# Kernel tuning notes

Measured on AMD Instinct MI355X. Metric: run time of the kernel, lower is better.

The kernel has to match this reference:

```python
import jax, jax.numpy as jnp
import numpy as np

EPS = 1e-06


def setup_inputs() -> dict:
    key = jax.random.key(0)
    k1, k2, k3 = jax.random.split(key, 3)
    B, H, S, D = 4, 16, 4096, 64
    query = jax.random.normal(k1, (B, H, S, D), dtype=jnp.float32)
    key_t = jax.random.normal(k2, (B, H, S, D), dtype=jnp.float32)
    value = jax.random.normal(k3, (B, H, S, D), dtype=jnp.float32)
    return {"query": query, "key": key_t, "value": value}


def _cosformer_features(x, cos_idx, sin_idx):
    # x: [B,H,S,D]; cos_idx/sin_idx: [S,1] -> features [B,H,S,2D]
    x_relu = jax.nn.relu(x)
    return jnp.concatenate([x_relu * cos_idx, x_relu * sin_idx], axis=-1)


def reference(query, key, value):
    B, H, S, D = query.shape
    query = query / jnp.sqrt(jnp.asarray(D, dtype=query.dtype))
    # idx = (pi/2) * [1..S]; angles divided by seq_len
    ang = (jnp.pi / 2) * jnp.arange(1, S + 1, dtype=query.dtype) / S  # [S]
    cos_idx = jnp.cos(ang)[:, None]  # [S,1]
    sin_idx = jnp.sin(ang)[:, None]  # [S,1]
    q_cs = _cosformer_features(query, cos_idx, sin_idx)  # [B,H,S,2D]
    k_cs = _cosformer_features(key, cos_idx, sin_idx)    # [B,H,S,2D]
    # norm: 1 / clamp(q_cs . sum_l(k_cs), eps)
    k_sum = jnp.sum(k_cs, axis=-2)  # [B,H,2D]
    norm = 1.0 / jnp.maximum(jnp.einsum('bhld,bhd->bhl', q_cs, k_sum), EPS)  # [B,H,S]
    # linear attention: KV aggregation then query projection
    kv = jnp.einsum('bhld,bhlm->bhdm', k_cs, value)  # [B,H,2D,D]
    out = jnp.einsum('bhld,bhdm->bhlm', q_cs, kv) * norm[..., None]  # [B,H,S,D]
    return out
```

## Files before the change

kernel.cpp:

```cpp
#include <hip/hip_runtime.h>
#include <hip/hip_bf16.h>
#include <math.h>

#define BHN    64
#define SEQ    4096
#define DIM    64
#define NCHUNK 8
#define CHUNK  (SEQ / NCHUNK)
#define KSTEP  64
#define NIT    (CHUNK / KSTEP)
#define KVF    (128 * DIM)
#define STRIDE_C ((size_t)BHN * KVF + (size_t)BHN * 128)
#define KSBASE ((size_t)BHN * KVF)
#define FRAGH  10240
#define LPAD   72

typedef __bf16 bf16x8v __attribute__((ext_vector_type(8)));
typedef float  f32x4v  __attribute__((ext_vector_type(4)));

__device__ inline f32x4v mfma16(bf16x8v a, bf16x8v b, f32x4v c) {
    return __builtin_amdgcn_mfma_f32_16x16x32_bf16(a, b, c, 0, 0, 0);
}

__device__ inline unsigned pk2(float a, float b) {
    __hip_bfloat162 t(__float2bfloat16(a), __float2bfloat16(b));
    return *(unsigned*)&t;
}

__device__ __forceinline__ void barrier_noflush() {
    asm volatile("s_waitcnt lgkmcnt(0)" ::: "memory");
    __builtin_amdgcn_s_barrier();
    asm volatile("" ::: "memory");
}

__device__ inline int swz(int d, int col) { return col ^ (4 * ((d >> 2) & 7)); }

template<int USE_ATOMIC>
__global__ __launch_bounds__(512, 2) void cosformer_kv_mfma(
    const float* __restrict__ K, const float* __restrict__ V,
    float* __restrict__ part)
{
    __shared__ ushort ktc[64][LPAD];
    __shared__ ushort kts[64][LPAD];
    __shared__ ushort vtt[64][LPAD];

    const int bh    = blockIdx.x / NCHUNK;
    const int chunk = blockIdx.x % NCHUNK;
    const int row0  = chunk * CHUNK;
    const float* Kb = K + (size_t)bh * SEQ * DIM;
    const float* Vb = V + (size_t)bh * SEQ * DIM;

    const int tid = threadIdx.x;
    const int dq = (tid & 15) * 4;
    const int g  = tid >> 4;
    const int lane = tid & 63;
    const int w    = tid >> 6;
    const int frow = lane & 15;
    const int kgrp = lane >> 4;

    f32x4v acc[5];
    #pragma unroll
    for (int t = 0; t < 5; ++t) acc[t] = (f32x4v){0.f, 0.f, 0.f, 0.f};

    bf16x8v onef;
    #pragma unroll
    for (int j = 0; j < 8; ++j) onef[j] = (frow == 0) ? (__bf16)1.0f : (__bf16)0.0f;

    float4 sA[4], sB[4], sC[4], sD[4], sE[4], sF[4], sG[4], sH[4];

    auto LOADS = [&](int it, float4* r) {
        const float* kp = Kb + (size_t)(row0 + it * KSTEP + 2 * g) * DIM + dq;
        const float* vp = Vb + (size_t)(row0 + it * KSTEP + 2 * g) * DIM + dq;
        r[0] = *(const float4*)kp;
        r[1] = *(const float4*)(kp + DIM);
        r[2] = *(const float4*)vp;
        r[3] = *(const float4*)(vp + DIM);
    };

    auto WRITES = [&](int it, const float4* r) {
        const int l0 = row0 + it * KSTEP + 2 * g;
        const float CC = 1.5707963267948966f / (float)SEQ;
        float s0v, c0, s1v, c1;
        __sincosf(CC * (float)(l0 + 1), &s0v, &c0);
        __sincosf(CC * (float)(l0 + 2), &s1v, &c1);
        float k0[4] = {r[0].x, r[0].y, r[0].z, r[0].w};
        float k1[4] = {r[1].x, r[1].y, r[1].z, r[1].w};
        float v0[4] = {r[2].x, r[2].y, r[2].z, r[2].w};
        float v1[4] = {r[3].x, r[3].y, r[3].z, r[3].w};
        #pragma unroll
        for (int i = 0; i < 4; ++i) {
            const int d = dq + i;
            const int c = swz(d, g);
            float r0 = fmaxf(k0[i], 0.f), r1 = fmaxf(k1[i], 0.f);
            ((unsigned*)&ktc[d][0])[c] = pk2(r0 * c0,  r1 * c1);
            ((unsigned*)&kts[d][0])[c] = pk2(r0 * s0v, r1 * s1v);
            ((unsigned*)&vtt[d][0])[c] = pk2(v0[i],    v1[i]);
        }
    };

    LOADS(0, sA); LOADS(1, sB); LOADS(2, sC); LOADS(3, sD);
    LOADS(4, sE); LOADS(5, sF); LOADS(6, sG); LOADS(7, sH);

    const int d0 = (w & 3) * 16 + frow;

    #pragma unroll
    for (int it = 0; it < NIT; ++it) {
        if      (it == 0) WRITES(0, sA);
        else if (it == 1) WRITES(1, sB);
        else if (it == 2) WRITES(2, sC);
        else if (it == 3) WRITES(3, sD);
        else if (it == 4) WRITES(4, sE);
        else if (it == 5) WRITES(5, sF);
        else if (it == 6) WRITES(6, sG);
        else              WRITES(7, sH);
        barrier_noflush();

        const ushort (*ap)[LPAD] = (w < 4) ? ktc : kts;
        #pragma unroll
        for (int ks = 0; ks < 2; ++ks) {
            const int cb = ks * 16 + kgrp * 4;
            bf16x8v a = *(const bf16x8v*)&ap[d0][2 * swz(d0, cb)];
            #pragma unroll
            for (int nt = 0; nt < 4; ++nt) {
                const int dn = nt * 16 + frow;
                bf16x8v b = *(const bf16x8v*)&vtt[dn][2 * swz(dn, cb)];
                acc[nt] = mfma16(a, b, acc[nt]);
            }
            acc[4] = mfma16(a, onef, acc[4]);
        }
        barrier_noflush();
    }

    const int fb = w * 16 + kgrp * 4;
    if (USE_ATOMIC) {
        float* pb = part + (size_t)bh * KVF;
        float* ps = part + KSBASE + bh * 128;
        #pragma unroll
        for (int nt = 0; nt < 4; ++nt)
            #pragma unroll
            for (int r = 0; r < 4; ++r)
                atomicAdd(&pb[(size_t)(fb + r) * DIM + nt * 16 + frow], acc[nt][r]);
        if (frow == 0)
            #pragma unroll
            for (int r = 0; r < 4; ++r) atomicAdd(&ps[fb + r], acc[4][r]);
    } else {
        float* pb = part + STRIDE_C * chunk + (size_t)bh * KVF;
        float* ps = part + STRIDE_C * chunk + KSBASE + bh * 128;
        #pragma unroll
        for (int nt = 0; nt < 4; ++nt)
            #pragma unroll
            for (int r = 0; r < 4; ++r)
                pb[(size_t)(fb + r) * DIM + nt * 16 + frow] = acc[nt][r];
        if (frow == 0)
            #pragma unroll
            for (int r = 0; r < 4; ++r) ps[fb + r] = acc[4][r];
    }
}

template<int NC>
__global__ __launch_bounds__(256) void reduce_pack(
    const float* __restrict__ part, __hip_bfloat16* __restrict__ bfrag)
{
    size_t o = (size_t)blockIdx.x * 256 + threadIdx.x;
    float s = 0.f;
    #pragma unroll
    for (int c = 0; c < NC; ++c) s += part[(size_t)c * STRIDE_C + o];
    if (o < KSBASE) {
        int head = (int)(o >> 13);
        int r = (int)(o & 8191);
        int k = r >> 6, n = r & 63;
        int t = n >> 4, ks = k >> 5, lg = (k >> 3) & 3, j = k & 7;
        int lane = lg * 16 + (n & 15);
        bfrag[(size_t)head * FRAGH + (size_t)(((t * 4 + ks) * 64 + lane) * 8 + j)] =
            __float2bfloat16(s);
    } else {
        int r = (int)(o - KSBASE);
        int head = r >> 7, k = r & 127;
        int ks = k >> 5, lg = (k >> 3) & 3, j = k & 7;
        bfrag[(size_t)head * FRAGH + (size_t)(((16 + ks) * 64 + lg * 16) * 8 + j)] =
            __float2bfloat16(s);
    }
}

__global__ __launch_bounds__(256) void cosformer_out_mfma(
    const float* __restrict__ Q, const __hip_bfloat16* __restrict__ bfrag,
    float* __restrict__ out)
{
    __shared__ __hip_bfloat16 sb[FRAGH];
    const int head = blockIdx.x >> 3;
    const int tile = blockIdx.x & 7;
    const int tid  = threadIdx.x;

    {
        const float4* src = (const float4*)(bfrag + (size_t)head * FRAGH);
        float4* dst = (float4*)sb;
        #pragma unroll
        for (int i = 0; i < 5; ++i) dst[tid + 256 * i] = src[tid + 256 * i];
    }

    const int lane = tid & 63;
    const int w    = tid >> 6;
    const int mrow = lane & 15;
    const int kgrp = lane >> 4;

    const float* Qb = Q + (size_t)head * SEQ * DIM;
    float*       Ob = out + (size_t)head * SEQ * DIM;
    const int rowblk = tile * 512;

    float4 qb[2][4];
    #pragma unroll
    for (int m = 0; m < 2; ++m) {
        const float4* qr = (const float4*)(Qb + (size_t)(rowblk + w * 32 + m * 16 + mrow) * DIM);
        qb[m][0] = qr[kgrp * 2];
        qb[m][1] = qr[kgrp * 2 + 1];
        qb[m][2] = qr[8 + kgrp * 2];
        qb[m][3] = qr[8 + kgrp * 2 + 1];
    }

    barrier_noflush();

    #pragma unroll
    for (int g = 0; g < 4; ++g) {
        const int base = rowblk + (g * 4 + w) * 32;

        bf16x8v af[2][4];
        #pragma unroll
        for (int m = 0; m < 2; ++m) {
            int arow = base + m * 16 + mrow;
            float ang = 1.5707963267948966f * (float)(arow + 1) / (float)SEQ;
            float sn, cn;
            __sincosf(ang, &sn, &cn);
            float crs = cn * 0.125f, srs = sn * 0.125f;
            float lo[8] = {qb[m][0].x, qb[m][0].y, qb[m][0].z, qb[m][0].w,
                           qb[m][1].x, qb[m][1].y, qb[m][1].z, qb[m][1].w};
            float hi[8] = {qb[m][2].x, qb[m][2].y, qb[m][2].z, qb[m][2].w,
                           qb[m][3].x, qb[m][3].y, qb[m][3].z, qb[m][3].w};
            #pragma unroll
            for (int j = 0; j < 8; ++j) {
                float rl = fmaxf(lo[j], 0.f);
                float rh = fmaxf(hi[j], 0.f);
                af[m][0][j] = (__bf16)(rl * crs);
                af[m][1][j] = (__bf16)(rh * crs);
                af[m][2][j] = (__bf16)(rl * srs);
                af[m][3][j] = (__bf16)(rh * srs);
            }
        }

        if (g < 3) {
            #pragma unroll
            for (int m = 0; m < 2; ++m) {
                const float4* qr = (const float4*)(Qb + (size_t)(rowblk + ((g + 1) * 4 + w) * 32 + m * 16 + mrow) * DIM);
                qb[m][0] = qr[kgrp * 2];
                qb[m][1] = qr[kgrp * 2 + 1];
                qb[m][2] = qr[8 + kgrp * 2];
                qb[m][3] = qr[8 + kgrp * 2 + 1];
            }
        }

        f32x4v acc[2][5];
        #pragma unroll
        for (int m = 0; m < 2; ++m)
            #pragma unroll
            for (int t = 0; t < 5; ++t)
                acc[m][t] = (f32x4v){0.f, 0.f, 0.f, 0.f};

        #pragma unroll
        for (int t = 0; t < 5; ++t)
            #pragma unroll
            for (int ks = 0; ks < 4; ++ks) {
                bf16x8v bf = *(const bf16x8v*)&sb[(size_t)(((t * 4 + ks) * 64 + lane) * 8)];
                acc[0][t] = mfma16(af[0][ks], bf, acc[0][t]);
                acc[1][t] = mfma16(af[1][ks], bf, acc[1][t]);
            }

        #pragma unroll
        for (int m = 0; m < 2; ++m) {
            #pragma unroll
            for (int r = 0; r < 4; ++r) {
                float den = __shfl(acc[m][4][r], lane & 48, 64);
                float invd = 1.0f / fmaxf(den, 1e-6f);
                int row = base + m * 16 + kgrp * 4 + r;
                float* op = Ob + (size_t)row * DIM + mrow;
                op[0]  = acc[m][0][r] * invd;
                op[16] = acc[m][1][r] * invd;
                op[32] = acc[m][2][r] * invd;
                op[48] = acc[m][3][r] * invd;
            }
        }
    }
}

extern "C" void kernel_launch(void* const* d_in, const int* in_sizes, int n_in,
                              void* d_out, int out_size, void* d_ws, size_t ws_size,
                              hipStream_t stream) {
    const float* Q = (const float*)d_in[0];
    const float* K = (const float*)d_in[1];
    const float* V = (const float*)d_in[2];
    float* out = (float*)d_out;
    float* ws  = (float*)d_ws;

    const size_t frag_bytes = (size_t)FRAGH * BHN * sizeof(__hip_bfloat16);
    const size_t need_full  = (size_t)NCHUNK * STRIDE_C * sizeof(float) + frag_bytes;

    if (ws_size >= need_full) {
        float* part = ws;
        __hip_bfloat16* bfrag = (__hip_bfloat16*)(ws + (size_t)NCHUNK * STRIDE_C);
        hipMemsetAsync(bfrag, 0, frag_bytes, stream);
        hipLaunchKernelGGL((cosformer_kv_mfma<0>), dim3(BHN * NCHUNK), dim3(512), 0, stream,
                           K, V, part);
        hipLaunchKernelGGL((reduce_pack<NCHUNK>), dim3((int)(STRIDE_C / 256)), dim3(256), 0, stream,
                           part, bfrag);
        hipLaunchKernelGGL(cosformer_out_mfma, dim3(BHN * 8), dim3(256), 0, stream,
                           Q, bfrag, out);
    } else {
        float* part = ws;
        __hip_bfloat16* bfrag = (__hip_bfloat16*)(ws + STRIDE_C);
        hipMemsetAsync(part, 0, STRIDE_C * sizeof(float), stream);
        hipMemsetAsync(bfrag, 0, frag_bytes, stream);
        hipLaunchKernelGGL((cosformer_kv_mfma<1>), dim3(BHN * NCHUNK), dim3(512), 0, stream,
                           K, V, part);
        hipLaunchKernelGGL((reduce_pack<1>), dim3((int)(STRIDE_C / 256)), dim3(256), 0, stream,
                           part, bfrag);
        hipLaunchKernelGGL(cosformer_out_mfma, dim3(BHN * 8), dim3(256), 0, stream,
                           Q, bfrag, out);
    }
}
```

Measured before the change: 76.82 us.

## Stage K/V tiles via async global-to-LDS loads with triple buffering

Replaces the register-prefetch of all eight 64-row K/V tiles with direct global_load_lds copies into a three-slot LDS ring of 32-row raw fp32 tiles, issued two iterations ahead. Half the threads now transform K into cos/sin features and half convert V, each into transposed bf16 LDS tiles. The loop is no longer unrolled, and the trailing barrier is dropped in favour of one barrier after staging and one after the transform. The aim is to cut register pressure and overlap the memory loads with compute. In exchange it uses much more LDS, halves the work per barrier, and drops the occupancy hint of two blocks per CU.

```diff
diff --git a/kernel.cpp b/kernel.cpp
--- a/kernel.cpp
+++ b/kernel.cpp
@@ -1,19 +1,20 @@
 #include <hip/hip_runtime.h>
 #include <hip/hip_bf16.h>
 #include <math.h>
+#include <stdint.h>
 
 #define BHN    64
 #define SEQ    4096
 #define DIM    64
 #define NCHUNK 8
 #define CHUNK  (SEQ / NCHUNK)
-#define KSTEP  64
+#define KSTEP  32
 #define NIT    (CHUNK / KSTEP)
 #define KVF    (128 * DIM)
 #define STRIDE_C ((size_t)BHN * KVF + (size_t)BHN * 128)
 #define KSBASE ((size_t)BHN * KVF)
 #define FRAGH  10240
-#define LPAD   72
+#define LPADT  40
 
 typedef __bf16 bf16x8v __attribute__((ext_vector_type(8)));
 typedef float  f32x4v  __attribute__((ext_vector_type(4)));
@@ -33,16 +34,23 @@
     asm volatile("" ::: "memory");
 }
 
-__device__ inline int swz(int d, int col) { return col ^ (4 * ((d >> 2) & 7)); }
+__device__ __forceinline__ void gload16(const float* g, const float* lds_base) {
+    __builtin_amdgcn_global_load_lds(
+        (const __attribute__((address_space(1))) void*)(uintptr_t)g,
+        (__attribute__((address_space(3)))  void*)(uintptr_t)lds_base,
+        16, 0, 0);
+}
 
 template<int USE_ATOMIC>
-__global__ __launch_bounds__(512, 2) void cosformer_kv_mfma(
+__global__ __launch_bounds__(512) void cosformer_kv_mfma(
     const float* __restrict__ K, const float* __restrict__ V,
     float* __restrict__ part)
 {
-    __shared__ ushort ktc[64][LPAD];
-    __shared__ ushort kts[64][LPAD];
-    __shared__ ushort vtt[64][LPAD];
+    __shared__ float  rawK[3][KSTEP][DIM];
+    __shared__ float  rawV[3][KSTEP][DIM];
+    __shared__ ushort ktc[DIM][LPADT];
+    __shared__ ushort kts[DIM][LPADT];
+    __shared__ ushort vtt[DIM][LPADT];
 
     const int bh    = blockIdx.x / NCHUNK;
     const int chunk = blockIdx.x % NCHUNK;
@@ -50,13 +58,15 @@
     const float* Kb = K + (size_t)bh * SEQ * DIM;
     const float* Vb = V + (size_t)bh * SEQ * DIM;
 
-    const int tid = threadIdx.x;
-    const int dq = (tid & 15) * 4;
-    const int g  = tid >> 4;
+    const int tid  = threadIdx.x;
     const int lane = tid & 63;
     const int w    = tid >> 6;
+    const int g2    = (tid >> 4) & 15;
+    const int dq    = (tid & 15) * 4;
+    const int kvsel = tid >> 8;
     const int frow = lane & 15;
     const int kgrp = lane >> 4;
+    const int d0   = (w & 3) * 16 + frow;
 
     f32x4v acc[5];
     #pragma unroll
@@ -66,69 +76,76 @@
     #pragma unroll
     for (int j = 0; j < 8; ++j) onef[j] = (frow == 0) ? (__bf16)1.0f : (__bf16)0.0f;
 
-    float4 sA[4], sB[4], sC[4], sD[4], sE[4], sF[4], sG[4], sH[4];
-
-    auto LOADS = [&](int it, float4* r) {
-        const float* kp = Kb + (size_t)(row0 + it * KSTEP + 2 * g) * DIM + dq;
-        const float* vp = Vb + (size_t)(row0 + it * KSTEP + 2 * g) * DIM + dq;
-        r[0] = *(const float4*)kp;
-        r[1] = *(const float4*)(kp + DIM);
-        r[2] = *(const float4*)vp;
-        r[3] = *(const float4*)(vp + DIM);
+    auto STAGE = [&](int it) {
+        const int buf = it % 3;
+        const size_t go = (size_t)(row0 + it * KSTEP) * DIM + w * 256 + lane * 4;
+        gload16(Kb + go, &rawK[buf][w * 4][0]);
+        gload16(Vb + go, &rawV[buf][w * 4][0]);
     };
 
-    auto WRITES = [&](int it, const float4* r) {
-        const int l0 = row0 + it * KSTEP + 2 * g;
-        const float CC = 1.5707963267948966f / (float)SEQ;
-        float s0v, c0, s1v, c1;
-        __sincosf(CC * (float)(l0 + 1), &s0v, &c0);
-        __sincosf(CC * (float)(l0 + 2), &s1v, &c1);
-        float k0[4] = {r[0].x, r[0].y, r[0].z, r[0].w};
-        float k1[4] = {r[1].x, r[1].y, r[1].z, r[1].w};
-        float v0[4] = {r[2].x, r[2].y, r[2].z, r[2].w};
-        float v1[4] = {r[3].x, r[3].y, r[3].z, r[3].w};
-        #pragma unroll
-        for (int i = 0; i < 4; ++i) {
-            const int d = dq + i;
-            const int c = swz(d, g);
-            float r0 = fmaxf(k0[i], 0.f), r1 = fmaxf(k1[i], 0.f);
-            ((unsigned*)&ktc[d][0])[c] = pk2(r0 * c0,  r1 * c1);
-            ((unsigned*)&kts[d][0])[c] = pk2(r0 * s0v, r1 * s1v);
-            ((unsigned*)&vtt[d][0])[c] = pk2(v0[i],    v1[i]);
+    auto TRANSFORM = [&](int it) {
+        const int buf = it % 3;
+        const int r = 2 * g2;
+        if (kvsel == 0) {
+            float4 k0 = *(const float4*)&rawK[buf][r][dq];
+            float4 k1 = *(const float4*)&rawK[buf][r + 1][dq];
+            const int l0 = row0 + it * KSTEP + r;
+            const float CC = 1.5707963267948966f / (float)SEQ;
+            float s0v, c0, s1v, c1;
+            __sincosf(CC * (float)(l0 + 1), &s0v, &c0);
+            __sincosf(CC * (float)(l0 + 2), &s1v, &c1);
+            float a0[4] = {k0.x, k0.y, k0.z, k0.w};
+            float a1[4] = {k1.x, k1.y, k1.z, k1.w};
+            #pragma unroll
+            for (int i = 0; i < 4; ++i) {
+                const int d = dq + i;
+                const int c = g2 ^ (4 * ((d >> 2) & 3));
+                float r0 = fmaxf(a0[i], 0.f), r1 = fmaxf(a1[i], 0.f);
+                ((unsigned*)&ktc[d][0])[c] = pk2(r0 * c0,  r1 * c1);
+                ((unsigned*)&kts[d][0])[c] = pk2(r0 * s0v, r1 * s1v);
+            }
+        } else {
+            float4 v0q = *(const float4*)&rawV[buf][r][dq];
+            float4 v1q = *(const float4*)&rawV[buf][r + 1][dq];
+            float a0[4] = {v0q.x, v0q.y, v0q.z, v0q.w};
+            float a1[4] = {v1q.x, v1q.y, v1q.z, v1q.w};
+            #pragma unroll
+            for (int i = 0; i < 4; ++i) {
+                const int d = dq + i;
+                const int c = g2 ^ (4 * ((d >> 2) & 3));
+                ((unsigned*)&vtt[d][0])[c] = pk2(a0[i], a1[i]);
+            }
         }
     };
 
-    LOADS(0, sA); LOADS(1, sB); LOADS(2, sC); LOADS(3, sD);
-    LOADS(4, sE); LOADS(5, sF); LOADS(6, sG); LOADS(7, sH);
-
-    const int d0 = (w & 3) * 16 + frow;
-
-    #pragma unroll
+    STAGE(0);
+    STAGE(1);
+
+    #pragma unroll 1
     for (int it = 0; it < NIT; ++it) {
-        if      (it == 0) WRITES(0, sA);
-        else if (it == 1) WRITES(1, sB);
-        else if (it == 2) WRITES(2, sC);
-        else if (it == 3) WRITES(3, sD);
-        else if (it == 4) WRITES(4, sE);
-        else if (it == 5) WRITES(5, sF);
-        else if (it == 6) WRITES(6, sG);
-        else              WRITES(7, sH);
+        if (it + 1 < NIT) asm volatile("s_waitcnt vmcnt(2)" ::: "memory");
+        else              asm volatile("s_waitcnt vmcnt(0)" ::: "memory");
+        __builtin_amdgcn_sched_barrier(0);
         barrier_noflush();
 
-        const ushort (*ap)[LPAD] = (w < 4) ? ktc : kts;
-        #pragma unroll
-        for (int ks = 0; ks < 2; ++ks) {
-            const int cb = ks * 16 + kgrp * 4;
-            bf16x8v a = *(const bf16x8v*)&ap[d0][2 * swz(d0, cb)];
+        if (it + 2 < NIT) STAGE(it + 2);
+
+        TRANSFORM(it);
+        barrier_noflush();
+
+        const ushort (*ap)[LPADT] = (w < 4) ? ktc : kts;
+        {
+            const int ca = (kgrp * 4) ^ (4 * ((d0 >> 2) & 3));
+            bf16x8v a = *(const bf16x8v*)&ap[d0][2 * ca];
             #pragma unroll
             for (int nt = 0; nt < 4; ++nt) {
                 const int dn = nt * 16 + frow;
-                bf16x8v b = *(const bf16x8v*)&vtt[dn][2 * swz(dn, cb)];
+                const int cb = (kgrp * 4) ^ (4 * ((dn >> 2) & 3));
+                bf16x8v b = *(const bf16x8v*)&vtt[dn][2 * cb];
                 acc[nt] = mfma16(a, b, acc[nt]);
             }
             acc[4] = mfma16(a, onef, acc[4]);
         }
-        barrier_noflush();
     }
 
     const int fb = w * 16 + kgrp * 4;
```

Result: faster. 71.63 us (-6.8%).

## Build KV MFMA fragments directly from global loads, dropping LDS transpose staging

Applied to the files above, without the earlier changes.

The KV aggregation kernel is rewritten so each wave loads K and V rows straight into MFMA operand registers and computes the cos and sin feature products and k-sums in registers. This removes the LDS transpose staging and the per-step block barriers. Each wave now owns 128 rows with a full 128x64 register accumulator. Pairs of waves merge through LDS and write 16 partial slots instead of 8, which doubles the partial-sum traffic that the reduce kernel must read. The strided scalar global loads and the higher register pressure may hurt memory coalescing and occupancy.

```diff
diff --git a/kernel.cpp b/kernel.cpp
--- a/kernel.cpp
+++ b/kernel.cpp
@@ -7,13 +7,11 @@
 #define DIM    64
 #define NCHUNK 8
 #define CHUNK  (SEQ / NCHUNK)
-#define KSTEP  64
-#define NIT    (CHUNK / KSTEP)
+#define NSLOT  16
 #define KVF    (128 * DIM)
 #define STRIDE_C ((size_t)BHN * KVF + (size_t)BHN * 128)
 #define KSBASE ((size_t)BHN * KVF)
 #define FRAGH  10240
-#define LPAD   72
 
 typedef __bf16 bf16x8v __attribute__((ext_vector_type(8)));
 typedef float  f32x4v  __attribute__((ext_vector_type(4)));
@@ -33,16 +31,12 @@
     asm volatile("" ::: "memory");
 }
 
-__device__ inline int swz(int d, int col) { return col ^ (4 * ((d >> 2) & 7)); }
-
 template<int USE_ATOMIC>
-__global__ __launch_bounds__(512, 2) void cosformer_kv_mfma(
+__global__ __launch_bounds__(256) void cosformer_kv_direct(
     const float* __restrict__ K, const float* __restrict__ V,
     float* __restrict__ part)
 {
-    __shared__ ushort ktc[64][LPAD];
-    __shared__ ushort kts[64][LPAD];
-    __shared__ ushort vtt[64][LPAD];
+    __shared__ float mbuf[130][64];
 
     const int bh    = blockIdx.x / NCHUNK;
     const int chunk = blockIdx.x % NCHUNK;
@@ -50,110 +44,151 @@
     const float* Kb = K + (size_t)bh * SEQ * DIM;
     const float* Vb = V + (size_t)bh * SEQ * DIM;
 
-    const int tid = threadIdx.x;
-    const int dq = (tid & 15) * 4;
-    const int g  = tid >> 4;
+    const int tid  = threadIdx.x;
     const int lane = tid & 63;
     const int w    = tid >> 6;
     const int frow = lane & 15;
     const int kgrp = lane >> 4;
 
-    f32x4v acc[5];
-    #pragma unroll
-    for (int t = 0; t < 5; ++t) acc[t] = (f32x4v){0.f, 0.f, 0.f, 0.f};
-
-    bf16x8v onef;
-    #pragma unroll
-    for (int j = 0; j < 8; ++j) onef[j] = (frow == 0) ? (__bf16)1.0f : (__bf16)0.0f;
-
-    float4 sA[4], sB[4], sC[4], sD[4], sE[4], sF[4], sG[4], sH[4];
-
-    auto LOADS = [&](int it, float4* r) {
-        const float* kp = Kb + (size_t)(row0 + it * KSTEP + 2 * g) * DIM + dq;
-        const float* vp = Vb + (size_t)(row0 + it * KSTEP + 2 * g) * DIM + dq;
-        r[0] = *(const float4*)kp;
-        r[1] = *(const float4*)(kp + DIM);
-        r[2] = *(const float4*)vp;
-        r[3] = *(const float4*)(vp + DIM);
-    };
-
-    auto WRITES = [&](int it, const float4* r) {
-        const int l0 = row0 + it * KSTEP + 2 * g;
-        const float CC = 1.5707963267948966f / (float)SEQ;
-        float s0v, c0, s1v, c1;
-        __sincosf(CC * (float)(l0 + 1), &s0v, &c0);
-        __sincosf(CC * (float)(l0 + 2), &s1v, &c1);
-        float k0[4] = {r[0].x, r[0].y, r[0].z, r[0].w};
-        float k1[4] = {r[1].x, r[1].y, r[1].z, r[1].w};
-        float v0[4] = {r[2].x, r[2].y, r[2].z, r[2].w};
-        float v1[4] = {r[3].x, r[3].y, r[3].z, r[3].w};
-        #pragma unroll
-        for (int i = 0; i < 4; ++i) {
-            const int d = dq + i;
-            const int c = swz(d, g);
-            float r0 = fmaxf(k0[i], 0.f), r1 = fmaxf(k1[i], 0.f);
-            ((unsigned*)&ktc[d][0])[c] = pk2(r0 * c0,  r1 * c1);
-            ((unsigned*)&kts[d][0])[c] = pk2(r0 * s0v, r1 * s1v);
-            ((unsigned*)&vtt[d][0])[c] = pk2(v0[i],    v1[i]);
-        }
-    };
-
-    LOADS(0, sA); LOADS(1, sB); LOADS(2, sC); LOADS(3, sD);
-    LOADS(4, sE); LOADS(5, sF); LOADS(6, sG); LOADS(7, sH);
-
-    const int d0 = (w & 3) * 16 + frow;
-
-    #pragma unroll
-    for (int it = 0; it < NIT; ++it) {
-        if      (it == 0) WRITES(0, sA);
-        else if (it == 1) WRITES(1, sB);
-        else if (it == 2) WRITES(2, sC);
-        else if (it == 3) WRITES(3, sD);
-        else if (it == 4) WRITES(4, sE);
-        else if (it == 5) WRITES(5, sF);
-        else if (it == 6) WRITES(6, sG);
-        else              WRITES(7, sH);
-        barrier_noflush();
-
-        const ushort (*ap)[LPAD] = (w < 4) ? ktc : kts;
-        #pragma unroll
-        for (int ks = 0; ks < 2; ++ks) {
-            const int cb = ks * 16 + kgrp * 4;
-            bf16x8v a = *(const bf16x8v*)&ap[d0][2 * swz(d0, cb)];
-            #pragma unroll
-            for (int nt = 0; nt < 4; ++nt) {
-                const int dn = nt * 16 + frow;
-                bf16x8v b = *(const bf16x8v*)&vtt[dn][2 * swz(dn, cb)];
-                acc[nt] = mfma16(a, b, acc[nt]);
-            }
-            acc[4] = mfma16(a, onef, acc[4]);
-        }
-        barrier_noflush();
-    }
-
-    const int fb = w * 16 + kgrp * 4;
+    f32x4v accC[4][4], accS[4][4];
+    #pragma unroll
+    for (int i = 0; i < 4; ++i)
+        #pragma unroll
+        for (int j = 0; j < 4; ++j) {
+            accC[i][j] = (f32x4v){0.f, 0.f, 0.f, 0.f};
+            accS[i][j] = (f32x4v){0.f, 0.f, 0.f, 0.f};
+        }
+    float ksc[4] = {0.f, 0.f, 0.f, 0.f};
+    float kss[4] = {0.f, 0.f, 0.f, 0.f};
+
+    const int wrow0 = row0 + w * 128;
+    const float CC = 1.5707963267948966f / (float)SEQ;
+
+    #pragma unroll 1
+    for (int st = 0; st < 4; ++st) {
+        const int sl = wrow0 + st * 32 + kgrp * 8;
+        const float* kp = Kb + (size_t)sl * DIM + frow;
+        const float* vp = Vb + (size_t)sl * DIM + frow;
+
+        float kraw[4][8], vraw[4][8];
+        #pragma unroll
+        for (int dq = 0; dq < 4; ++dq)
+            #pragma unroll
+            for (int j = 0; j < 8; ++j)
+                kraw[dq][j] = kp[(size_t)j * DIM + dq * 16];
+        #pragma unroll
+        for (int nq = 0; nq < 4; ++nq)
+            #pragma unroll
+            for (int j = 0; j < 8; ++j)
+                vraw[nq][j] = vp[(size_t)j * DIM + nq * 16];
+
+        float cs_[8], sn_[8];
+        #pragma unroll
+        for (int j = 0; j < 8; ++j)
+            __sincosf(CC * (float)(sl + j + 1), &sn_[j], &cs_[j]);
+
+        union U { bf16x8v v; unsigned u[4]; };
+        U bv[4];
+        #pragma unroll
+        for (int nq = 0; nq < 4; ++nq)
+            #pragma unroll
+            for (int i2 = 0; i2 < 4; ++i2)
+                bv[nq].u[i2] = pk2(vraw[nq][2 * i2], vraw[nq][2 * i2 + 1]);
+
+        #pragma unroll
+        for (int dq = 0; dq < 4; ++dq) {
+            U ac, as2;
+            #pragma unroll
+            for (int i2 = 0; i2 < 4; ++i2) {
+                float r0 = fmaxf(kraw[dq][2 * i2],     0.f);
+                float r1 = fmaxf(kraw[dq][2 * i2 + 1], 0.f);
+                ac.u[i2]  = pk2(r0 * cs_[2 * i2], r1 * cs_[2 * i2 + 1]);
+                as2.u[i2] = pk2(r0 * sn_[2 * i2], r1 * sn_[2 * i2 + 1]);
+            }
+            #pragma unroll
+            for (int j = 0; j < 8; ++j) {
+                float rr = fmaxf(kraw[dq][j], 0.f);
+                ksc[dq] += rr * cs_[j];
+                kss[dq] += rr * sn_[j];
+            }
+            #pragma unroll
+            for (int nq = 0; nq < 4; ++nq) {
+                accC[dq][nq] = mfma16(ac.v,  bv[nq].v, accC[dq][nq]);
+                accS[dq][nq] = mfma16(as2.v, bv[nq].v, accS[dq][nq]);
+            }
+        }
+    }
+
+    #pragma unroll
+    for (int dq = 0; dq < 4; ++dq) {
+        ksc[dq] += __shfl_xor(ksc[dq], 16); ksc[dq] += __shfl_xor(ksc[dq], 32);
+        kss[dq] += __shfl_xor(kss[dq], 16); kss[dq] += __shfl_xor(kss[dq], 32);
+    }
+
     if (USE_ATOMIC) {
         float* pb = part + (size_t)bh * KVF;
         float* ps = part + KSBASE + bh * 128;
         #pragma unroll
-        for (int nt = 0; nt < 4; ++nt)
-            #pragma unroll
-            for (int r = 0; r < 4; ++r)
-                atomicAdd(&pb[(size_t)(fb + r) * DIM + nt * 16 + frow], acc[nt][r]);
-        if (frow == 0)
-            #pragma unroll
-            for (int r = 0; r < 4; ++r) atomicAdd(&ps[fb + r], acc[4][r]);
-    } else {
-        float* pb = part + STRIDE_C * chunk + (size_t)bh * KVF;
-        float* ps = part + STRIDE_C * chunk + KSBASE + bh * 128;
-        #pragma unroll
-        for (int nt = 0; nt < 4; ++nt)
-            #pragma unroll
-            for (int r = 0; r < 4; ++r)
-                pb[(size_t)(fb + r) * DIM + nt * 16 + frow] = acc[nt][r];
-        if (frow == 0)
-            #pragma unroll
-            for (int r = 0; r < 4; ++r) ps[fb + r] = acc[4][r];
+        for (int dq = 0; dq < 4; ++dq) {
+            #pragma unroll
+            for (int nq = 0; nq < 4; ++nq)
+                #pragma unroll
+                for (int r = 0; r < 4; ++r) {
+                    int f = dq * 16 + kgrp * 4 + r;
+                    atomicAdd(&pb[(size_t)f * DIM + nq * 16 + frow], accC[dq][nq][r]);
+                    atomicAdd(&pb[(size_t)(f + 64) * DIM + nq * 16 + frow], accS[dq][nq][r]);
+                }
+            if (kgrp == 0) {
+                atomicAdd(&ps[dq * 16 + frow], ksc[dq]);
+                atomicAdd(&ps[64 + dq * 16 + frow], kss[dq]);
+            }
+        }
+        return;
+    }
+
+    #pragma unroll
+    for (int half = 0; half < 2; ++half) {
+        if (w == 2 * half) {
+            #pragma unroll
+            for (int dq = 0; dq < 4; ++dq)
+                #pragma unroll
+                for (int nq = 0; nq < 4; ++nq)
+                    #pragma unroll
+                    for (int r = 0; r < 4; ++r) {
+                        int f = dq * 16 + kgrp * 4 + r;
+                        mbuf[f][nq * 16 + frow]      = accC[dq][nq][r];
+                        mbuf[f + 64][nq * 16 + frow] = accS[dq][nq][r];
+                    }
+            if (kgrp == 0)
+                #pragma unroll
+                for (int dq = 0; dq < 4; ++dq) {
+                    mbuf[128][dq * 16 + frow] = ksc[dq];
+                    mbuf[129][dq * 16 + frow] = kss[dq];
+                }
+        }
+        __syncthreads();
+        if (w == 2 * half + 1) {
+            float* pb = part + STRIDE_C * (size_t)(chunk * 2 + half) + (size_t)bh * KVF;
+            float* ps = part + STRIDE_C * (size_t)(chunk * 2 + half) + KSBASE + bh * 128;
+            #pragma unroll
+            for (int dq = 0; dq < 4; ++dq) {
+                #pragma unroll
+                for (int nq = 0; nq < 4; ++nq)
+                    #pragma unroll
+                    for (int r = 0; r < 4; ++r) {
+                        int f = dq * 16 + kgrp * 4 + r;
+                        pb[(size_t)f * DIM + nq * 16 + frow] =
+                            accC[dq][nq][r] + mbuf[f][nq * 16 + frow];
+                        pb[(size_t)(f + 64) * DIM + nq * 16 + frow] =
+                            accS[dq][nq][r] + mbuf[f + 64][nq * 16 + frow];
+                    }
+                if (kgrp == 0) {
+                    ps[dq * 16 + frow]      = ksc[dq] + mbuf[128][dq * 16 + frow];
+                    ps[64 + dq * 16 + frow] = kss[dq] + mbuf[129][dq * 16 + frow];
+                }
+            }
+        }
+        __syncthreads();
     }
 }
 
@@ -300,15 +335,15 @@
     float* ws  = (float*)d_ws;
 
     const size_t frag_bytes = (size_t)FRAGH * BHN * sizeof(__hip_bfloat16);
-    const size_t need_full  = (size_t)NCHUNK * STRIDE_C * sizeof(float) + frag_bytes;
+    const size_t need_full  = (size_t)NSLOT * STRIDE_C * sizeof(float) + frag_bytes;
 
     if (ws_size >= need_full) {
         float* part = ws;
-        __hip_bfloat16* bfrag = (__hip_bfloat16*)(ws + (size_t)NCHUNK * STRIDE_C);
+        __hip_bfloat16* bfrag = (__hip_bfloat16*)(ws + (size_t)NSLOT * STRIDE_C);
         hipMemsetAsync(bfrag, 0, frag_bytes, stream);
-        hipLaunchKernelGGL((cosformer_kv_mfma<0>), dim3(BHN * NCHUNK), dim3(512), 0, stream,
+        hipLaunchKernelGGL((cosformer_kv_direct<0>), dim3(BHN * NCHUNK), dim3(256), 0, stream,
                            K, V, part);
-        hipLaunchKernelGGL((reduce_pack<NCHUNK>), dim3((int)(STRIDE_C / 256)), dim3(256), 0, stream,
+        hipLaunchKernelGGL((reduce_pack<NSLOT>), dim3((int)(STRIDE_C / 256)), dim3(256), 0, stream,
                            part, bfrag);
         hipLaunchKernelGGL(cosformer_out_mfma, dim3(BHN * 8), dim3(256), 0, stream,
                            Q, bfrag, out);
@@ -317,7 +352,7 @@
         __hip_bfloat16* bfrag = (__hip_bfloat16*)(ws + STRIDE_C);
         hipMemsetAsync(part, 0, STRIDE_C * sizeof(float), stream);
         hipMemsetAsync(bfrag, 0, frag_bytes, stream);
-        hipLaunchKernelGGL((cosformer_kv_mfma<1>), dim3(BHN * NCHUNK), dim3(512), 0, stream,
+        hipLaunchKernelGGL((cosformer_kv_direct<1>), dim3(BHN * NCHUNK), dim3(256), 0, stream,
                            K, V, part);
         hipLaunchKernelGGL((reduce_pack<1>), dim3((int)(STRIDE_C / 256)), dim3(256), 0, stream,
                            part, bfrag);
```

Result: slower. 89.02 us (+15.9%).
